# Optimization experiments

Hardware: AMD Instinct MI355X
Metric: run time of the kernel (lower is better)

Reference implementation:

```python
import jax, jax.numpy as jnp
import numpy as np

N_NODES = 50000
N_EDGES = 800000
IN_DIM_NODE = 128
IN_DIM_EDGE = 16
OUT_DIM = 32
N_HEAD = 4


def setup_inputs() -> dict:
    key = jax.random.key(0)
    ks = jax.random.split(key, 8)
    feats_node = jax.random.normal(ks[0], (N_NODES, IN_DIM_NODE), dtype=jnp.float32)
    feats_edge = jax.random.normal(ks[1], (N_EDGES, IN_DIM_EDGE), dtype=jnp.float32)
    src = jax.random.randint(ks[2], (N_EDGES,), 0, N_NODES)
    dst = jax.random.randint(ks[3], (N_EDGES,), 0, N_NODES)
    # params: init normal(std=0.5) as in the torch module
    W_node = 0.5 * jax.random.normal(ks[4], (N_HEAD * OUT_DIM, IN_DIM_NODE), dtype=jnp.float32)
    attn_l = 0.5 * jax.random.normal(ks[5], (N_HEAD, OUT_DIM), dtype=jnp.float32)
    attn_r = 0.5 * jax.random.normal(ks[6], (N_HEAD, OUT_DIM), dtype=jnp.float32)
    attn_e = 0.5 * jax.random.normal(ks[7], (N_HEAD, IN_DIM_EDGE), dtype=jnp.float32)
    return {"feats_node": feats_node, "feats_edge": feats_edge, "src": src,
            "dst": dst, "W_node": W_node, "attn_l": attn_l, "attn_r": attn_r,
            "attn_e": attn_e}


def reference(feats_node, feats_edge, src, dst, W_node, attn_l, attn_r, attn_e):
    N = feats_node.shape[0]
    H, D = attn_l.shape
    # node projection: [N, H, D]
    feat_n = (feats_node @ W_node.T).reshape(N, H, D)
    # per-node attention logits: [N, H]
    el = jnp.einsum('nhd,hd->nh', feat_n, attn_l)
    er = jnp.einsum('nhd,hd->nh', feat_n, attn_r)
    # per-edge (edge-feature) logit: [E, H]
    ee = jnp.einsum('ef,hf->eh', feats_edge, attn_e)
    # gather logits along edges and apply leaky relu (slope 0.2)
    e = jax.nn.leaky_relu(el[src] + er[dst] + ee, negative_slope=0.2)  # [E, H]
    # edge softmax segmented by destination node (numerically stable)
    m = jax.ops.segment_max(e, dst, num_segments=N)          # [N, H]
    m = jnp.where(jnp.isfinite(m), m, 0.0)                   # guard 0-degree nodes
    e_exp = jnp.exp(e - m[dst])                               # [E, H]
    s = jax.ops.segment_sum(e_exp, dst, num_segments=N)       # [N, H]
    a = e_exp / s[dst]                                        # [E, H]
    # weighted scatter-aggregate: sum over in-edges of a * ft[src]
    msg = feat_n[src] * a[:, :, None]                          # [E, H, D]
    out = jax.ops.segment_sum(msg, dst, num_segments=N)       # [N, H, D]
    return out.reshape(N, H * D)
```

## Files before the change

### kernel.cpp

```cpp
#include <hip/hip_runtime.h>
#include <hip/hip_bf16.h>
#include <math.h>

#define NN 50000
#define NE 800000
#define SCAN_NB ((NN + 255) / 256)
#define PROJ_NBLK 512
#define PROJ_RPB ((NN + PROJ_NBLK - 1) / PROJ_NBLK)

__global__ void k_hist(const int* __restrict__ dst, int* __restrict__ count) {
    int e = blockIdx.x * 256 + threadIdx.x;
    if (e < NE) atomicAdd(&count[dst[e]], 1);
}

__global__ __launch_bounds__(256) void k_scan_a(const int* __restrict__ count,
                                                int* __restrict__ pre,
                                                int* __restrict__ bsum) {
    __shared__ int buf[256];
    int t = threadIdx.x;
    int gid = blockIdx.x * 256 + t;
    int v = (gid < NN) ? count[gid] : 0;
    int x = v;
    buf[t] = x;
    __syncthreads();
    for (int off = 1; off < 256; off <<= 1) {
        int add = (t >= off) ? buf[t - off] : 0;
        __syncthreads();
        x += add;
        buf[t] = x;
        __syncthreads();
    }
    if (gid < NN) pre[gid] = x - v;
    if (t == 255) bsum[blockIdx.x] = x;
}

__global__ __launch_bounds__(256) void k_scan_b(const int* __restrict__ bsum,
                                                int* __restrict__ bofs) {
    __shared__ int buf[256];
    int t = threadIdx.x;
    int v = (t < SCAN_NB) ? bsum[t] : 0;
    int x = v;
    buf[t] = x;
    __syncthreads();
    for (int off = 1; off < 256; off <<= 1) {
        int add = (t >= off) ? buf[t - off] : 0;
        __syncthreads();
        x += add;
        buf[t] = x;
        __syncthreads();
    }
    if (t < SCAN_NB) bofs[t] = x - v;
    if (t == 255) bofs[SCAN_NB] = x;
}

__global__ __launch_bounds__(256) void k_scan_c(int* __restrict__ pre,
                                                const int* __restrict__ bofs,
                                                int* __restrict__ cursor) {
    int gid = blockIdx.x * 256 + threadIdx.x;
    if (gid < NN) {
        int val = pre[gid] + bofs[gid >> 8];
        pre[gid] = val;
        cursor[gid] = val;
    }
    if (gid == 0) pre[NN] = bofs[SCAN_NB];
}

__global__ __launch_bounds__(256) void k_proj3(
    const float* __restrict__ X, const float* __restrict__ W,
    const float* __restrict__ al, const float* __restrict__ ar,
    __hip_bfloat16* __restrict__ FB, float* __restrict__ el, float* __restrict__ er)
{
    __shared__ float Xs[16 * 128];
    const int t = threadIdx.x;
    const int w = t >> 6, l = t & 63;
    const int c = w * 32 + (l & 31);
    const int kh = (l >> 5) * 64;

    float4 wreg[16];
#pragma unroll
    for (int j = 0; j < 16; ++j)
        wreg[j] = *reinterpret_cast<const float4*>(W + (size_t)c * 128 + kh + j * 4);

    const float alv = al[c], arv = ar[c];
    const int rowLo = blockIdx.x * PROJ_RPB;
    const int rowHi = (rowLo + PROJ_RPB < NN) ? rowLo + PROJ_RPB : NN;

    for (int r0 = rowLo; r0 < rowHi; r0 += 16) {
        __syncthreads();
#pragma unroll
        for (int i = 0; i < 2; ++i) {
            int idx = t + i * 256;
            int rr = idx >> 5, c4 = (idx & 31) * 4;
            int r = r0 + rr;
            float4 v = make_float4(0.f, 0.f, 0.f, 0.f);
            if (r < NN) v = *reinterpret_cast<const float4*>(X + (size_t)r * 128 + c4);
            *reinterpret_cast<float4*>(&Xs[rr * 128 + c4]) = v;
        }
        __syncthreads();
        int nr = rowHi - r0; if (nr > 16) nr = 16;
        for (int rr = 0; rr < nr; ++rr) {
            const float4* xp = reinterpret_cast<const float4*>(&Xs[rr * 128 + kh]);
            float a0 = 0.f, a1 = 0.f, a2 = 0.f, a3 = 0.f;
#pragma unroll
            for (int j = 0; j < 16; ++j) {
                float4 x = xp[j];
                a0 += x.x * wreg[j].x; a1 += x.y * wreg[j].y;
                a2 += x.z * wreg[j].z; a3 += x.w * wreg[j].w;
            }
            float tot = (a0 + a1) + (a2 + a3);
            tot += __shfl_xor(tot, 32);
            int row = r0 + rr;
            if (l < 32) FB[(size_t)row * 128 + c] = __float2bfloat16(tot);
            float pl = tot * alv, pr = tot * arv;
#pragma unroll
            for (int off = 16; off; off >>= 1) {
                pl += __shfl_xor(pl, off);
                pr += __shfl_xor(pr, off);
            }
            if (l == 0) { el[row * 4 + w] = pl; er[row * 4 + w] = pr; }
        }
    }
}

__global__ void k_logits_fill(const float* __restrict__ FE, const int* __restrict__ src,
                              const int* __restrict__ dst, const float* __restrict__ ae,
                              const float* __restrict__ el, const float* __restrict__ er,
                              int* __restrict__ cursor, float4* __restrict__ lsort,
                              int* __restrict__ ssort) {
    int e = blockIdx.x * 256 + threadIdx.x;
    if (e >= NE) return;
    float fe[16];
#pragma unroll
    for (int i = 0; i < 4; ++i) {
        float4 v = *reinterpret_cast<const float4*>(FE + (size_t)e * 16 + i * 4);
        fe[i * 4 + 0] = v.x; fe[i * 4 + 1] = v.y; fe[i * 4 + 2] = v.z; fe[i * 4 + 3] = v.w;
    }
    int s = src[e], d = dst[e];
    float4 elv = *reinterpret_cast<const float4*>(el + (size_t)s * 4);
    float4 erv = *reinterpret_cast<const float4*>(er + (size_t)d * 4);
    float base[4] = {elv.x + erv.x, elv.y + erv.y, elv.z + erv.z, elv.w + erv.w};
    float o[4];
#pragma unroll
    for (int h = 0; h < 4; ++h) {
        float ee = 0.f;
#pragma unroll
        for (int i = 0; i < 16; ++i) ee += fe[i] * ae[h * 16 + i];
        float v = base[h] + ee;
        o[h] = v > 0.f ? v : 0.2f * v;
    }
    int pos = atomicAdd(&cursor[d], 1);
    lsort[pos] = make_float4(o[0], o[1], o[2], o[3]);
    ssort[pos] = s;
}

__global__ __launch_bounds__(256) void k_aggr3(
    const __hip_bfloat16* __restrict__ FB, const float* __restrict__ lsf,
    const int* __restrict__ ssort, const int* __restrict__ row_ptr,
    float* __restrict__ out)
{
    int wid = threadIdx.x >> 6, lane = threadIdx.x & 63;
    int node = blockIdx.x * 4 + wid;
    if (node >= NN) return;
    int s0 = row_ptr[node], s1 = row_ptr[node + 1];
    int q = lane & 15, p = lane >> 4;
    float4* o4 = reinterpret_cast<float4*>(out + (size_t)node * 128);
    if (s1 == s0) {
        if (p == 0) {
            o4[2 * q]     = make_float4(0.f, 0.f, 0.f, 0.f);
            o4[2 * q + 1] = make_float4(0.f, 0.f, 0.f, 0.f);
        }
        return;
    }
    const float4* lsort = reinterpret_cast<const float4*>(lsf);

    bool have = (s0 + lane) < s1;
    float4 my = have ? lsort[s0 + lane] : make_float4(-1e30f, -1e30f, -1e30f, -1e30f);
    float m0 = my.x, m1 = my.y, m2 = my.z, m3 = my.w;
    for (int i = s0 + lane + 64; i < s1; i += 64) {
        float4 lg = lsort[i];
        m0 = fmaxf(m0, lg.x); m1 = fmaxf(m1, lg.y);
        m2 = fmaxf(m2, lg.z); m3 = fmaxf(m3, lg.w);
    }
#pragma unroll
    for (int off = 32; off; off >>= 1) {
        m0 = fmaxf(m0, __shfl_xor(m0, off)); m1 = fmaxf(m1, __shfl_xor(m1, off));
        m2 = fmaxf(m2, __shfl_xor(m2, off)); m3 = fmaxf(m3, __shfl_xor(m3, off));
    }
    float t0 = have ? __expf(my.x - m0) : 0.f;
    float t1 = have ? __expf(my.y - m1) : 0.f;
    float t2 = have ? __expf(my.z - m2) : 0.f;
    float t3 = have ? __expf(my.w - m3) : 0.f;
    for (int i = s0 + lane + 64; i < s1; i += 64) {
        float4 lg = lsort[i];
        t0 += __expf(lg.x - m0); t1 += __expf(lg.y - m1);
        t2 += __expf(lg.z - m2); t3 += __expf(lg.w - m3);
    }
#pragma unroll
    for (int off = 32; off; off >>= 1) {
        t0 += __shfl_xor(t0, off); t1 += __shfl_xor(t1, off);
        t2 += __shfl_xor(t2, off); t3 += __shfl_xor(t3, off);
    }

    int ha = q >> 2;
    float mh = (ha == 0) ? m0 : (ha == 1) ? m1 : (ha == 2) ? m2 : m3;
    float sh = (ha == 0) ? t0 : (ha == 1) ? t1 : (ha == 2) ? t2 : t3;
    float rh = 1.f / sh;
    const unsigned short* FBu = reinterpret_cast<const unsigned short*>(FB);
    float c0 = 0.f, c1 = 0.f, c2 = 0.f, c3 = 0.f, c4 = 0.f, c5 = 0.f, c6 = 0.f, c7 = 0.f;
    for (int it = s0; it < s1; it += 4) {
        int i = it + p;
        if (i < s1) {
            int sv = ssort[i];
            float lg = lsf[(size_t)i * 4 + ha];
            float wgt = __expf(lg - mh) * rh;
            uint4 f = *reinterpret_cast<const uint4*>(FBu + (size_t)sv * 128 + q * 8);
            c0 += wgt * __uint_as_float(f.x << 16);
            c1 += wgt * __uint_as_float(f.x & 0xffff0000u);
            c2 += wgt * __uint_as_float(f.y << 16);
            c3 += wgt * __uint_as_float(f.y & 0xffff0000u);
            c4 += wgt * __uint_as_float(f.z << 16);
            c5 += wgt * __uint_as_float(f.z & 0xffff0000u);
            c6 += wgt * __uint_as_float(f.w << 16);
            c7 += wgt * __uint_as_float(f.w & 0xffff0000u);
        }
    }
#pragma unroll
    for (int off = 16; off <= 32; off <<= 1) {
        c0 += __shfl_xor(c0, off); c1 += __shfl_xor(c1, off);
        c2 += __shfl_xor(c2, off); c3 += __shfl_xor(c3, off);
        c4 += __shfl_xor(c4, off); c5 += __shfl_xor(c5, off);
        c6 += __shfl_xor(c6, off); c7 += __shfl_xor(c7, off);
    }
    if (p == 0) {
        o4[2 * q]     = make_float4(c0, c1, c2, c3);
        o4[2 * q + 1] = make_float4(c4, c5, c6, c7);
    }
}

extern "C" void kernel_launch(void* const* d_in, const int* in_sizes, int n_in,
                              void* d_out, int out_size, void* d_ws, size_t ws_size,
                              hipStream_t stream) {
    const float* feats_node = (const float*)d_in[0];
    const float* feats_edge = (const float*)d_in[1];
    const int*   src        = (const int*)d_in[2];
    const int*   dst        = (const int*)d_in[3];
    const float* W          = (const float*)d_in[4];
    const float* al         = (const float*)d_in[5];
    const float* ar         = (const float*)d_in[6];
    const float* ae         = (const float*)d_in[7];
    float* out = (float*)d_out;

    char* ws = (char*)d_ws;
    size_t off = 0;
    __hip_bfloat16* feat_b = (__hip_bfloat16*)(ws + off); off += (size_t)NN * 128 * 2;
    float* el     = (float*)(ws + off); off += (size_t)NN * 4 * 4;
    float* er     = (float*)(ws + off); off += (size_t)NN * 4 * 4;
    float* lsort  = (float*)(ws + off); off += (size_t)NE * 4 * 4;
    int* ssort    = (int*)(ws + off);   off += (size_t)NE * 4;
    int* count    = (int*)(ws + off);   off += (size_t)NN * 4;
    int* row_ptr  = (int*)(ws + off);   off += (size_t)(NN + 16) * 4;
    int* cursor   = (int*)(ws + off);   off += (size_t)NN * 4;
    int* bsum     = (int*)(ws + off);   off += (size_t)(SCAN_NB + 16) * 4;
    int* bofs     = (int*)(ws + off);   off += (size_t)(SCAN_NB + 16) * 4;

    hipMemsetAsync(count, 0, (size_t)NN * 4, stream);

    k_hist<<<(NE + 255) / 256, 256, 0, stream>>>(dst, count);
    k_scan_a<<<SCAN_NB, 256, 0, stream>>>(count, row_ptr, bsum);
    k_scan_b<<<1, 256, 0, stream>>>(bsum, bofs);
    k_scan_c<<<SCAN_NB, 256, 0, stream>>>(row_ptr, bofs, cursor);
    k_proj3<<<PROJ_NBLK, 256, 0, stream>>>(feats_node, W, al, ar, feat_b, el, er);
    k_logits_fill<<<(NE + 255) / 256, 256, 0, stream>>>(feats_edge, src, dst, ae, el, er,
                                                        cursor, (float4*)lsort, ssort);
    k_aggr3<<<(NN + 3) / 4, 256, 0, stream>>>(feat_b, lsort, ssort, row_ptr, out);
}
```

Measured before the change: 323.5 us.

## Fold attention vectors into weights, split projection, cache softmax weights in LDS

Precomputes W^T·attn_l/attn_r so per-node el/er become a small 128x8 matvec in a separate kernel, removing the per-row shuffle reductions from the projection kernel. The projection kernel is restructured to one 32-row tile per block with a larger grid. The aggregation kernel stores exp weights in LDS for nodes with degree ≤64 and processes two edges per iteration, avoiding recomputing exp and rereading logits. The extra kernel rereads node features, adding memory traffic.

```diff
diff --git a/kernel.cpp b/kernel.cpp
--- a/kernel.cpp
+++ b/kernel.cpp
@@ -5,8 +5,118 @@
 #define NN 50000
 #define NE 800000
 #define SCAN_NB ((NN + 255) / 256)
-#define PROJ_NBLK 512
-#define PROJ_RPB ((NN + PROJ_NBLK - 1) / PROJ_NBLK)
+#define PROJ_NBLK ((NN + 31) / 32)
+#define ELR_NBLK ((NN + 31) / 32)
+
+__global__ __launch_bounds__(256) void k_prep(const float* __restrict__ W,
+                                              const float* __restrict__ al,
+                                              const float* __restrict__ ar,
+                                              float* __restrict__ vlr) {
+    int t = threadIdx.x;
+    int hlr = t >> 5;
+    int k4 = t & 31;
+    int h = hlr & 3;
+    const float* a = (hlr & 4) ? ar : al;
+    float4 acc = make_float4(0.f, 0.f, 0.f, 0.f);
+    for (int d = 0; d < 32; ++d) {
+        float av = a[h * 32 + d];
+        float4 wv = *reinterpret_cast<const float4*>(W + (size_t)(h * 32 + d) * 128 + k4 * 4);
+        acc.x += av * wv.x; acc.y += av * wv.y;
+        acc.z += av * wv.z; acc.w += av * wv.w;
+    }
+    *reinterpret_cast<float4*>(vlr + hlr * 128 + k4 * 4) = acc;
+}
+
+__global__ __launch_bounds__(256) void k_elr(const float* __restrict__ X,
+                                             const float* __restrict__ vlr,
+                                             float* __restrict__ elr) {
+    __shared__ float vs[8 * 128];
+    int t = threadIdx.x;
+    for (int i = t; i < 1024; i += 256) vs[i] = vlr[i];
+    __syncthreads();
+    int lane = t & 63, wave = t >> 6;
+    int grp = lane >> 3;
+    int j = lane & 7;
+    int node = blockIdx.x * 32 + wave * 8 + grp;
+    float a0 = 0.f, a1 = 0.f, a2 = 0.f, a3 = 0.f, a4 = 0.f, a5 = 0.f, a6 = 0.f, a7 = 0.f;
+    if (node < NN) {
+        const float4* xp = reinterpret_cast<const float4*>(X + (size_t)node * 128 + j * 16);
+#pragma unroll
+        for (int s = 0; s < 4; ++s) {
+            float4 xv = xp[s];
+            const float* vb = &vs[j * 16 + s * 4];
+            float4 v0 = *reinterpret_cast<const float4*>(vb + 0 * 128);
+            float4 v1 = *reinterpret_cast<const float4*>(vb + 1 * 128);
+            float4 v2 = *reinterpret_cast<const float4*>(vb + 2 * 128);
+            float4 v3 = *reinterpret_cast<const float4*>(vb + 3 * 128);
+            float4 v4 = *reinterpret_cast<const float4*>(vb + 4 * 128);
+            float4 v5 = *reinterpret_cast<const float4*>(vb + 5 * 128);
+            float4 v6 = *reinterpret_cast<const float4*>(vb + 6 * 128);
+            float4 v7 = *reinterpret_cast<const float4*>(vb + 7 * 128);
+            a0 += xv.x * v0.x + xv.y * v0.y + xv.z * v0.z + xv.w * v0.w;
+            a1 += xv.x * v1.x + xv.y * v1.y + xv.z * v1.z + xv.w * v1.w;
+            a2 += xv.x * v2.x + xv.y * v2.y + xv.z * v2.z + xv.w * v2.w;
+            a3 += xv.x * v3.x + xv.y * v3.y + xv.z * v3.z + xv.w * v3.w;
+            a4 += xv.x * v4.x + xv.y * v4.y + xv.z * v4.z + xv.w * v4.w;
+            a5 += xv.x * v5.x + xv.y * v5.y + xv.z * v5.z + xv.w * v5.w;
+            a6 += xv.x * v6.x + xv.y * v6.y + xv.z * v6.z + xv.w * v6.w;
+            a7 += xv.x * v7.x + xv.y * v7.y + xv.z * v7.z + xv.w * v7.w;
+        }
+    }
+#pragma unroll
+    for (int off = 1; off <= 4; off <<= 1) {
+        a0 += __shfl_xor(a0, off); a1 += __shfl_xor(a1, off);
+        a2 += __shfl_xor(a2, off); a3 += __shfl_xor(a3, off);
+        a4 += __shfl_xor(a4, off); a5 += __shfl_xor(a5, off);
+        a6 += __shfl_xor(a6, off); a7 += __shfl_xor(a7, off);
+    }
+    float outv = (j == 0) ? a0 : (j == 1) ? a1 : (j == 2) ? a2 : (j == 3) ? a3
+               : (j == 4) ? a4 : (j == 5) ? a5 : (j == 6) ? a6 : a7;
+    if (node < NN) elr[(size_t)node * 8 + j] = outv;
+}
+
+__global__ __launch_bounds__(256) void k_proj4(const float* __restrict__ X,
+                                               const float* __restrict__ W,
+                                               __hip_bfloat16* __restrict__ FB) {
+    __shared__ float Xs[32 * 128];
+    const int t = threadIdx.x;
+    const int w = t >> 6, l = t & 63;
+    const int c = w * 32 + (l & 31);
+    const int kh = (l >> 5) * 64;
+
+    float4 wreg[16];
+#pragma unroll
+    for (int j = 0; j < 16; ++j)
+        wreg[j] = *reinterpret_cast<const float4*>(W + (size_t)c * 128 + kh + j * 4);
+
+    const int r0 = blockIdx.x * 32;
+#pragma unroll
+    for (int i = 0; i < 4; ++i) {
+        int idx = t + i * 256;
+        int rr = idx >> 5, c4 = (idx & 31) * 4;
+        int r = r0 + rr;
+        float4 v = make_float4(0.f, 0.f, 0.f, 0.f);
+        if (r < NN) v = *reinterpret_cast<const float4*>(X + (size_t)r * 128 + c4);
+        *reinterpret_cast<float4*>(&Xs[rr * 128 + c4]) = v;
+    }
+    __syncthreads();
+
+#pragma unroll 2
+    for (int rr = 0; rr < 32; ++rr) {
+        const float4* xp = reinterpret_cast<const float4*>(&Xs[rr * 128 + kh]);
+        float a0 = 0.f, a1 = 0.f, a2 = 0.f, a3 = 0.f;
+#pragma unroll
+        for (int j = 0; j < 16; ++j) {
+            float4 x = xp[j];
+            a0 += x.x * wreg[j].x; a1 += x.y * wreg[j].y;
+            a2 += x.z * wreg[j].z; a3 += x.w * wreg[j].w;
+        }
+        float tot = (a0 + a1) + (a2 + a3);
+        tot += __shfl_xor(tot, 32);
+        int row = r0 + rr;
+        if (l < 32 && row < NN) FB[(size_t)row * 128 + c] = __float2bfloat16(tot);
+    }
+}
 
 __global__ void k_hist(const int* __restrict__ dst, int* __restrict__ count) {
     int e = blockIdx.x * 256 + threadIdx.x;
@@ -65,68 +175,10 @@
     if (gid == 0) pre[NN] = bofs[SCAN_NB];
 }
 
-__global__ __launch_bounds__(256) void k_proj3(
-    const float* __restrict__ X, const float* __restrict__ W,
-    const float* __restrict__ al, const float* __restrict__ ar,
-    __hip_bfloat16* __restrict__ FB, float* __restrict__ el, float* __restrict__ er)
-{
-    __shared__ float Xs[16 * 128];
-    const int t = threadIdx.x;
-    const int w = t >> 6, l = t & 63;
-    const int c = w * 32 + (l & 31);
-    const int kh = (l >> 5) * 64;
-
-    float4 wreg[16];
-#pragma unroll
-    for (int j = 0; j < 16; ++j)
-        wreg[j] = *reinterpret_cast<const float4*>(W + (size_t)c * 128 + kh + j * 4);
-
-    const float alv = al[c], arv = ar[c];
-    const int rowLo = blockIdx.x * PROJ_RPB;
-    const int rowHi = (rowLo + PROJ_RPB < NN) ? rowLo + PROJ_RPB : NN;
-
-    for (int r0 = rowLo; r0 < rowHi; r0 += 16) {
-        __syncthreads();
-#pragma unroll
-        for (int i = 0; i < 2; ++i) {
-            int idx = t + i * 256;
-            int rr = idx >> 5, c4 = (idx & 31) * 4;
-            int r = r0 + rr;
-            float4 v = make_float4(0.f, 0.f, 0.f, 0.f);
-            if (r < NN) v = *reinterpret_cast<const float4*>(X + (size_t)r * 128 + c4);
-            *reinterpret_cast<float4*>(&Xs[rr * 128 + c4]) = v;
-        }
-        __syncthreads();
-        int nr = rowHi - r0; if (nr > 16) nr = 16;
-        for (int rr = 0; rr < nr; ++rr) {
-            const float4* xp = reinterpret_cast<const float4*>(&Xs[rr * 128 + kh]);
-            float a0 = 0.f, a1 = 0.f, a2 = 0.f, a3 = 0.f;
-#pragma unroll
-            for (int j = 0; j < 16; ++j) {
-                float4 x = xp[j];
-                a0 += x.x * wreg[j].x; a1 += x.y * wreg[j].y;
-                a2 += x.z * wreg[j].z; a3 += x.w * wreg[j].w;
-            }
-            float tot = (a0 + a1) + (a2 + a3);
-            tot += __shfl_xor(tot, 32);
-            int row = r0 + rr;
-            if (l < 32) FB[(size_t)row * 128 + c] = __float2bfloat16(tot);
-            float pl = tot * alv, pr = tot * arv;
-#pragma unroll
-            for (int off = 16; off; off >>= 1) {
-                pl += __shfl_xor(pl, off);
-                pr += __shfl_xor(pr, off);
-            }
-            if (l == 0) { el[row * 4 + w] = pl; er[row * 4 + w] = pr; }
-        }
-    }
-}
-
 __global__ void k_logits_fill(const float* __restrict__ FE, const int* __restrict__ src,
                               const int* __restrict__ dst, const float* __restrict__ ae,
-                              const float* __restrict__ el, const float* __restrict__ er,
-                              int* __restrict__ cursor, float4* __restrict__ lsort,
-                              int* __restrict__ ssort) {
+                              const float* __restrict__ elr, int* __restrict__ cursor,
+                              float4* __restrict__ lsort, int* __restrict__ ssort) {
     int e = blockIdx.x * 256 + threadIdx.x;
     if (e >= NE) return;
     float fe[16];
@@ -136,8 +188,8 @@
         fe[i * 4 + 0] = v.x; fe[i * 4 + 1] = v.y; fe[i * 4 + 2] = v.z; fe[i * 4 + 3] = v.w;
     }
     int s = src[e], d = dst[e];
-    float4 elv = *reinterpret_cast<const float4*>(el + (size_t)s * 4);
-    float4 erv = *reinterpret_cast<const float4*>(er + (size_t)d * 4);
+    float4 elv = *reinterpret_cast<const float4*>(elr + (size_t)s * 8);
+    float4 erv = *reinterpret_cast<const float4*>(elr + (size_t)d * 8 + 4);
     float base[4] = {elv.x + erv.x, elv.y + erv.y, elv.z + erv.z, elv.w + erv.w};
     float o[4];
 #pragma unroll
@@ -153,11 +205,12 @@
     ssort[pos] = s;
 }
 
-__global__ __launch_bounds__(256) void k_aggr3(
+__global__ __launch_bounds__(256) void k_aggr4(
     const __hip_bfloat16* __restrict__ FB, const float* __restrict__ lsf,
     const int* __restrict__ ssort, const int* __restrict__ row_ptr,
     float* __restrict__ out)
 {
+    __shared__ float wex[4][64 * 4];
     int wid = threadIdx.x >> 6, lane = threadIdx.x & 63;
     int node = blockIdx.x * 4 + wid;
     if (node >= NN) return;
@@ -172,6 +225,8 @@
         return;
     }
     const float4* lsort = reinterpret_cast<const float4*>(lsf);
+    const int deg = s1 - s0;
+    const bool small = deg <= 64;
 
     bool have = (s0 + lane) < s1;
     float4 my = have ? lsort[s0 + lane] : make_float4(-1e30f, -1e30f, -1e30f, -1e30f);
@@ -190,38 +245,65 @@
     float t1 = have ? __expf(my.y - m1) : 0.f;
     float t2 = have ? __expf(my.z - m2) : 0.f;
     float t3 = have ? __expf(my.w - m3) : 0.f;
+    if (small && have)
+        *reinterpret_cast<float4*>(&wex[wid][lane * 4]) = make_float4(t0, t1, t2, t3);
+    float u0 = t0, u1 = t1, u2 = t2, u3 = t3;
     for (int i = s0 + lane + 64; i < s1; i += 64) {
         float4 lg = lsort[i];
-        t0 += __expf(lg.x - m0); t1 += __expf(lg.y - m1);
-        t2 += __expf(lg.z - m2); t3 += __expf(lg.w - m3);
+        u0 += __expf(lg.x - m0); u1 += __expf(lg.y - m1);
+        u2 += __expf(lg.z - m2); u3 += __expf(lg.w - m3);
     }
 #pragma unroll
     for (int off = 32; off; off >>= 1) {
-        t0 += __shfl_xor(t0, off); t1 += __shfl_xor(t1, off);
-        t2 += __shfl_xor(t2, off); t3 += __shfl_xor(t3, off);
+        u0 += __shfl_xor(u0, off); u1 += __shfl_xor(u1, off);
+        u2 += __shfl_xor(u2, off); u3 += __shfl_xor(u3, off);
     }
 
     int ha = q >> 2;
     float mh = (ha == 0) ? m0 : (ha == 1) ? m1 : (ha == 2) ? m2 : m3;
-    float sh = (ha == 0) ? t0 : (ha == 1) ? t1 : (ha == 2) ? t2 : t3;
+    float sh = (ha == 0) ? u0 : (ha == 1) ? u1 : (ha == 2) ? u2 : u3;
     float rh = 1.f / sh;
     const unsigned short* FBu = reinterpret_cast<const unsigned short*>(FB);
     float c0 = 0.f, c1 = 0.f, c2 = 0.f, c3 = 0.f, c4 = 0.f, c5 = 0.f, c6 = 0.f, c7 = 0.f;
-    for (int it = s0; it < s1; it += 4) {
-        int i = it + p;
-        if (i < s1) {
-            int sv = ssort[i];
-            float lg = lsf[(size_t)i * 4 + ha];
-            float wgt = __expf(lg - mh) * rh;
-            uint4 f = *reinterpret_cast<const uint4*>(FBu + (size_t)sv * 128 + q * 8);
-            c0 += wgt * __uint_as_float(f.x << 16);
-            c1 += wgt * __uint_as_float(f.x & 0xffff0000u);
-            c2 += wgt * __uint_as_float(f.y << 16);
-            c3 += wgt * __uint_as_float(f.y & 0xffff0000u);
-            c4 += wgt * __uint_as_float(f.z << 16);
-            c5 += wgt * __uint_as_float(f.z & 0xffff0000u);
-            c6 += wgt * __uint_as_float(f.w << 16);
-            c7 += wgt * __uint_as_float(f.w & 0xffff0000u);
+    if (small) {
+        asm volatile("s_waitcnt lgkmcnt(0)" ::: "memory");
+        for (int it = s0; it < s1; it += 8) {
+            int i0 = it + p, i1 = it + 4 + p;
+            bool b0 = i0 < s1, b1 = i1 < s1;
+            int sv0 = b0 ? ssort[i0] : 0;
+            int sv1 = b1 ? ssort[i1] : 0;
+            uint4 f0 = b0 ? *reinterpret_cast<const uint4*>(FBu + (size_t)sv0 * 128 + q * 8)
+                          : make_uint4(0, 0, 0, 0);
+            uint4 f1 = b1 ? *reinterpret_cast<const uint4*>(FBu + (size_t)sv1 * 128 + q * 8)
+                          : make_uint4(0, 0, 0, 0);
+            float w0 = b0 ? wex[wid][(i0 - s0) * 4 + ha] * rh : 0.f;
+            float w1 = b1 ? wex[wid][(i1 - s0) * 4 + ha] * rh : 0.f;
+            c0 += w0 * __uint_as_float(f0.x << 16) + w1 * __uint_as_float(f1.x << 16);
+            c1 += w0 * __uint_as_float(f0.x & 0xffff0000u) + w1 * __uint_as_float(f1.x & 0xffff0000u);
+            c2 += w0 * __uint_as_float(f0.y << 16) + w1 * __uint_as_float(f1.y << 16);
+            c3 += w0 * __uint_as_float(f0.y & 0xffff0000u) + w1 * __uint_as_float(f1.y & 0xffff0000u);
+            c4 += w0 * __uint_as_float(f0.z << 16) + w1 * __uint_as_float(f1.z << 16);
+            c5 += w0 * __uint_as_float(f0.z & 0xffff0000u) + w1 * __uint_as_float(f1.z & 0xffff0000u);
+            c6 += w0 * __uint_as_float(f0.w << 16) + w1 * __uint_as_float(f1.w << 16);
+            c7 += w0 * __uint_as_float(f0.w & 0xffff0000u) + w1 * __uint_as_float(f1.w & 0xffff0000u);
+        }
+    } else {
+        for (int it = s0; it < s1; it += 4) {
+            int i = it + p;
+            if (i < s1) {
+                int sv = ssort[i];
+                float lg = lsf[(size_t)i * 4 + ha];
+                float wgt = __expf(lg - mh) * rh;
+                uint4 f = *reinterpret_cast<const uint4*>(FBu + (size_t)sv * 128 + q * 8);
+                c0 += wgt * __uint_as_float(f.x << 16);
+                c1 += wgt * __uint_as_float(f.x & 0xffff0000u);
+                c2 += wgt * __uint_as_float(f.y << 16);
+                c3 += wgt * __uint_as_float(f.y & 0xffff0000u);
+                c4 += wgt * __uint_as_float(f.z << 16);
+                c5 += wgt * __uint_as_float(f.z & 0xffff0000u);
+                c6 += wgt * __uint_as_float(f.w << 16);
+                c7 += wgt * __uint_as_float(f.w & 0xffff0000u);
+            }
         }
     }
 #pragma unroll
@@ -253,8 +335,8 @@
     char* ws = (char*)d_ws;
     size_t off = 0;
     __hip_bfloat16* feat_b = (__hip_bfloat16*)(ws + off); off += (size_t)NN * 128 * 2;
-    float* el     = (float*)(ws + off); off += (size_t)NN * 4 * 4;
-    float* er     = (float*)(ws + off); off += (size_t)NN * 4 * 4;
+    float* elr    = (float*)(ws + off); off += (size_t)NN * 8 * 4;
+    float* vlr    = (float*)(ws + off); off += (size_t)8 * 128 * 4;
     float* lsort  = (float*)(ws + off); off += (size_t)NE * 4 * 4;
     int* ssort    = (int*)(ws + off);   off += (size_t)NE * 4;
     int* count    = (int*)(ws + off);   off += (size_t)NN * 4;
@@ -269,8 +351,10 @@
     k_scan_a<<<SCAN_NB, 256, 0, stream>>>(count, row_ptr, bsum);
     k_scan_b<<<1, 256, 0, stream>>>(bsum, bofs);
     k_scan_c<<<SCAN_NB, 256, 0, stream>>>(row_ptr, bofs, cursor);
-    k_proj3<<<PROJ_NBLK, 256, 0, stream>>>(feats_node, W, al, ar, feat_b, el, er);
-    k_logits_fill<<<(NE + 255) / 256, 256, 0, stream>>>(feats_edge, src, dst, ae, el, er,
+    k_prep<<<1, 256, 0, stream>>>(W, al, ar, vlr);
+    k_elr<<<ELR_NBLK, 256, 0, stream>>>(feats_node, vlr, elr);
+    k_proj4<<<PROJ_NBLK, 256, 0, stream>>>(feats_node, W, feat_b);
+    k_logits_fill<<<(NE + 255) / 256, 256, 0, stream>>>(feats_edge, src, dst, ae, elr,
                                                         cursor, (float4*)lsort, ssort);
-    k_aggr3<<<(NN + 3) / 4, 256, 0, stream>>>(feat_b, lsort, ssort, row_ptr, out);
-}
+    k_aggr4<<<(NN + 3) / 4, 256, 0, stream>>>(feat_b, lsort, ssort, row_ptr, out);
+}
```

Result: faster. 304.5 us (-5.9%).
